# Kernel tuning notes

Hardware: AMD Instinct MI355X
Metric: run time of the kernel (lower is better)

The kernel has to match this reference:

```python
import jax, jax.numpy as jnp
import numpy as np

TOPK, NUM_CLASSES, ALPHA, BETA, EPS = 13, 80, 1.0, 6.0, 1e-9
IOU_EPS = 1e-7  # eps used inside bbox_iou (ultralytics default)


def ciou(box1, box2):
    # box1, box2: broadcastable [..., 4] in xyxy format; returns CIoU [..., 1]
    b1x1, b1y1, b1x2, b1y2 = jnp.split(box1, 4, axis=-1)
    b2x1, b2y1, b2x2, b2y2 = jnp.split(box2, 4, axis=-1)
    w1, h1 = b1x2 - b1x1, b1y2 - b1y1 + IOU_EPS
    w2, h2 = b2x2 - b2x1, b2y2 - b2y1 + IOU_EPS
    inter = (jnp.clip(jnp.minimum(b1x2, b2x2) - jnp.maximum(b1x1, b2x1), 0.0) *
             jnp.clip(jnp.minimum(b1y2, b2y2) - jnp.maximum(b1y1, b2y1), 0.0))
    union = w1 * h1 + w2 * h2 - inter + IOU_EPS
    iou = inter / union
    cw = jnp.maximum(b1x2, b2x2) - jnp.minimum(b1x1, b2x1)  # enclosing box width
    ch = jnp.maximum(b1y2, b2y2) - jnp.minimum(b1y1, b2y1)
    c2 = cw ** 2 + ch ** 2 + IOU_EPS
    rho2 = ((b2x1 + b2x2 - b1x1 - b1x2) ** 2 + (b2y1 + b2y2 - b1y1 - b1y2) ** 2) / 4.0
    v = (4.0 / np.pi ** 2) * (jnp.arctan(w2 / h2) - jnp.arctan(w1 / h1)) ** 2
    alpha = jax.lax.stop_gradient(v / (v - iou + (1.0 + IOU_EPS)))  # torch: with no_grad
    return iou - (rho2 / c2 + v * alpha)


def tal_forward(pd_scores, pd_bboxes, anc_points, gt_labels, gt_bboxes, mask_gt):
    bs, na, nc = pd_scores.shape
    nb = gt_bboxes.shape[1]
    dt = pd_scores.dtype
    mgt = mask_gt[..., 0]  # (b, nb)

    # --- select_candidates_in_gts: anchor center strictly inside gt box ---
    lt, rb = gt_bboxes[..., :2], gt_bboxes[..., 2:]
    deltas = jnp.concatenate([anc_points[None, None, :, :] - lt[:, :, None, :],
                              rb[:, :, None, :] - anc_points[None, None, :, :]], axis=-1)  # (b,nb,na,4)
    mask_in_gts = (deltas.min(-1) > EPS).astype(dt)  # (b,nb,na)
    valid = (mask_in_gts * mgt[:, :, None]) > 0  # bool (b,nb,na)

    # --- get_box_metrics: class score gather + pairwise CIoU, masked ---
    lbl = gt_labels[..., 0].astype(jnp.int32)  # (b,nb)
    scores = jnp.take_along_axis(pd_scores, lbl[:, None, :], axis=2)  # (b,na,nb)
    bbox_scores = jnp.where(valid, scores.transpose(0, 2, 1), 0.0)  # (b,nb,na)
    ov = ciou(gt_bboxes[:, :, None, :], pd_bboxes[:, None, :, :])[..., 0]  # (b,nb,na)
    overlaps = jnp.where(valid, jnp.clip(ov, 0.0), 0.0)
    align_metric = bbox_scores ** ALPHA * overlaps ** BETA

    # --- select_topk_candidates ---
    _, tk_i = jax.lax.top_k(align_metric, TOPK)  # (b,nb,TOPK)
    tk_i = jnp.where(mgt[:, :, None] > 0, tk_i, 0)  # invalid gt rows -> all idx 0 (counted >1 -> zeroed)
    flat_i = tk_i.reshape(bs * nb, TOPK)
    cnt = jnp.zeros((bs * nb, na), jnp.int32).at[jnp.arange(bs * nb)[:, None], flat_i].add(1)
    cnt = cnt.reshape(bs, nb, na)
    is_in_topk = jnp.where(cnt > 1, 0, cnt).astype(dt)
    mask_pos = is_in_topk * mask_in_gts * mgt[:, :, None]

    # --- select_highest_overlaps: resolve anchors claimed by multiple gts ---
    fg = mask_pos.sum(-2)  # (b,na)
    mask_multi = fg[:, None, :] > 1
    max_idx = overlaps.argmax(1)  # (b,na)
    is_max = jax.nn.one_hot(max_idx, nb, dtype=dt).transpose(0, 2, 1)  # (b,nb,na)
    mask_pos = jnp.where(mask_multi, is_max, mask_pos)
    fg_mask = mask_pos.sum(-2)  # (b,na)
    target_gt_idx = mask_pos.argmax(-2)  # (b,na)

    # --- get_targets ---
    flat_gt_idx = target_gt_idx + jnp.arange(bs)[:, None] * nb  # (b,na)
    target_labels = jnp.clip(lbl.reshape(-1)[flat_gt_idx], 0)
    target_bboxes = gt_bboxes.reshape(-1, 4)[flat_gt_idx]  # (b,na,4)
    target_scores = jax.nn.one_hot(target_labels, nc, dtype=dt)
    target_scores = jnp.where(fg_mask[..., None] > 0, target_scores, 0.0)

    # --- normalization of align metric ---
    align_metric = align_metric * mask_pos
    pos_align = align_metric.max(-1, keepdims=True)  # (b,nb,1)
    pos_over = (overlaps * mask_pos).max(-1, keepdims=True)
    norm = (align_metric * pos_over / (pos_align + EPS)).max(-2)[..., None]  # (b,na,1)
    target_scores = target_scores * norm
    return target_labels, target_bboxes, target_scores, fg_mask > 0, target_gt_idx


def _make_boxes(key, shape):
    kc, kw = jax.random.split(key)
    c = jax.random.uniform(kc, shape[:-1] + (2,), jnp.float32, 60.0, 580.0)
    wh = jax.random.uniform(kw, shape[:-1] + (2,), jnp.float32, 20.0, 120.0)
    return jnp.concatenate([c - wh / 2, c + wh / 2], axis=-1)


def setup_inputs() -> dict:
    key = jax.random.key(0)
    ks = jax.random.split(key, 6)
    bs, na, nc, nb = 32, 8400, 80, 64
    pd_scores = jax.random.uniform(ks[0], (bs, na, nc), jnp.float32)
    pd_bboxes = _make_boxes(ks[1], (bs, na, 4))
    anc_points = jax.random.uniform(ks[2], (na, 2), jnp.float32, 0.0, 640.0)
    gt_labels = jax.random.randint(ks[3], (bs, nb, 1), 0, nc, dtype=jnp.int32)
    gt_bboxes = _make_boxes(ks[4], (bs, nb, 4))
    mask_gt = (jax.random.uniform(ks[5], (bs, nb, 1)) < 0.8).astype(jnp.float32)
    return {"pd_scores": pd_scores, "pd_bboxes": pd_bboxes, "anc_points": anc_points,
            "gt_labels": gt_labels, "gt_bboxes": gt_bboxes, "mask_gt": mask_gt}


def reference(pd_scores, pd_bboxes, anc_points, gt_labels, gt_bboxes, mask_gt):
    return tal_forward(pd_scores, pd_bboxes, anc_points, gt_labels, gt_bboxes, mask_gt)
```

## Files before the change

### kernel.cpp

```cpp
#include <hip/hip_runtime.h>
#include <stdint.h>

#pragma clang fp contract(off)

#define BS 32
#define NB 64
#define NA 8400
#define NC 80
#define TK 13
#define QCAP 640
#define CMAX (QCAP + 32)
#define FORCED 32

typedef float floatx4 __attribute__((ext_vector_type(4)));

__device__ __forceinline__ float ciou_f(float g0, float g1, float g2, float g3,
                                        float p0, float p1, float p2, float p3) {
    const float E = 1e-7f;
    float w1 = g2 - g0, h1 = (g3 - g1) + E;
    float w2 = p2 - p0, h2 = (p3 - p1) + E;
    float iw = fminf(g2, p2) - fmaxf(g0, p0); iw = fmaxf(iw, 0.f);
    float ih = fminf(g3, p3) - fmaxf(g1, p1); ih = fmaxf(ih, 0.f);
    float inter = iw * ih;
    float uni = w1 * h1 + w2 * h2 - inter + E;
    float iou = inter / uni;
    float cw = fmaxf(g2, p2) - fminf(g0, p0);
    float ch = fmaxf(g3, p3) - fminf(g1, p1);
    float c2 = cw * cw + ch * ch + E;
    float dx = p0 + p2 - g0 - g2;
    float dy = p1 + p3 - g1 - g3;
    float rho2 = (dx * dx + dy * dy) / 4.0f;
    float da = atanf(w2 / h2) - atanf(w1 / h1);
    float v = 0.4052847345693511f * (da * da);
    float alpha = v / ((v - iou) + 1.0000001f);
    return iou - (rho2 / c2 + v * alpha);
}

__global__ __launch_bounds__(256) void k1a_scan(
    const float* __restrict__ anc,
    const float* __restrict__ gt_bboxes,
    const float* __restrict__ mask_gt,
    int* __restrict__ qcnt, int* __restrict__ qlist)
{
    int b = blockIdx.y;
    int a = blockIdx.x * 256 + threadIdx.x;
    int lane = threadIdx.x & 63;
    bool inrange = a < NA;
    float2 ap = inrange ? *(const float2*)&anc[2 * a] : make_float2(-1.f, -1.f);
    for (int j = 0; j < NB; j++) {
        int r = b * NB + j;
        float mg = mask_gt[r];
        float4 g = *(const float4*)&gt_bboxes[r * 4];
        float d0 = ap.x - g.x, d1 = ap.y - g.y, d2 = g.z - ap.x, d3 = g.w - ap.y;
        float dmin = fminf(fminf(d0, d1), fminf(d2, d3));
        bool hit = inrange && (mg > 0.f) && (dmin > 1e-9f);
        unsigned long long m = __ballot(hit);
        if (m) {
            int rank = __popcll(m & ((1ull << lane) - 1ull));
            int ldr = __ffsll((long long)m) - 1;
            int base = 0;
            if (lane == ldr) base = atomicAdd(&qcnt[r], __popcll(m));
            base = __shfl(base, ldr);
            int p = base + rank;
            if (hit && p < QCAP) qlist[r * QCAP + p] = a;
        }
    }
}

__global__ __launch_bounds__(64) void k1b_topk(
    const float* __restrict__ pd_scores,
    const float* __restrict__ pd_bboxes,
    const float* __restrict__ anc,
    const int* __restrict__ gt_labels,
    const float* __restrict__ gt_bboxes,
    const float* __restrict__ mask_gt,
    const int* __restrict__ qcnt, const int* __restrict__ qlist,
    int* __restrict__ tk_a, float* __restrict__ tk_v,
    float* __restrict__ tk_o, int* __restrict__ tk_f,
    int* __restrict__ cnt)
{
    int r = blockIdx.x;
    int b = r >> 6;
    int lane = threadIdx.x;

    if (mask_gt[r] <= 0.f) {
        if (lane < TK) {
            tk_a[r * TK + lane] = 0; tk_v[r * TK + lane] = 0.f;
            tk_o[r * TK + lane] = 0.f; tk_f[r * TK + lane] = 0;
        }
        return;
    }

    __shared__ int   ca[CMAX];
    __shared__ float cv[CMAX];
    __shared__ float co[CMAX];

    float4 g = *(const float4*)&gt_bboxes[r * 4];
    int lbl = gt_labels[r];
    int n0 = min(qcnt[r], QCAP);

    bool add = false;
    if (lane < FORCED) {
        float2 ap = *(const float2*)&anc[2 * lane];
        float d0 = ap.x - g.x, d1 = ap.y - g.y, d2 = g.z - ap.x, d3 = g.w - ap.y;
        float dmin = fminf(fminf(d0, d1), fminf(d2, d3));
        add = !(dmin > 1e-9f);
    }
    unsigned long long mb = __ballot(add);
    int pos = __popcll(mb & ((1ull << lane) - 1ull));
    if (add) { ca[n0 + pos] = lane; cv[n0 + pos] = 0.f; co[n0 + pos] = 0.f; }
    int n = n0 + __popcll(mb);

    for (int c = lane; c < n0; c += 64) {
        int a = qlist[r * QCAP + c];
        float4 p = *(const float4*)&pd_bboxes[(b * NA + a) * 4];
        float ov = fmaxf(ciou_f(g.x, g.y, g.z, g.w, p.x, p.y, p.z, p.w), 0.f);
        float sc = pd_scores[(b * NA + a) * NC + lbl];
        float o2 = ov * ov;
        ca[c] = a | (1 << 30); cv[c] = sc * (o2 * o2 * o2); co[c] = ov;
    }
    __syncthreads();

    unsigned consumed = 0;
    int wslot = 0; float wval = 0.f;
    for (int round = 0; round < TK; round++) {
        float bv = -2.f; int bgi = 0x7fffffff; int bsl = 0;
        int li = 0;
        for (int c = lane; c < n; c += 64, li++) {
            if (consumed & (1u << li)) continue;
            float v = cv[c]; int gi = ca[c] & 0x3fffffff;
            if (v > bv || (v == bv && gi < bgi)) { bv = v; bgi = gi; bsl = c; }
        }
        for (int off = 32; off; off >>= 1) {
            float v2 = __shfl_down(bv, off);
            int  gi2 = __shfl_down(bgi, off);
            int  sl2 = __shfl_down(bsl, off);
            if (v2 > bv || (v2 == bv && gi2 < bgi)) { bv = v2; bgi = gi2; bsl = sl2; }
        }
        int wsl = __shfl(bsl, 0);
        float wv = __shfl(bv, 0);
        if ((wsl & 63) == lane) consumed |= 1u << (wsl >> 6);
        if (lane == round) { wslot = wsl; wval = wv; }
    }
    if (lane < TK) {
        int packed = ca[wslot]; int a = packed & 0x3fffffff; int in = (packed >> 30) & 1;
        tk_a[r * TK + lane] = a;
        tk_v[r * TK + lane] = wval;
        tk_o[r * TK + lane] = co[wslot];
        tk_f[r * TK + lane] = in;
        if (in) atomicAdd(&cnt[b * NA + a], 1);
    }
}

__global__ void k2c_single(const int* __restrict__ tk_a, const float* __restrict__ tk_v,
                           const float* __restrict__ tk_o, const int* __restrict__ tk_f,
                           const int* __restrict__ cnt, int* __restrict__ jA,
                           float* __restrict__ av,
                           unsigned* __restrict__ posA, unsigned* __restrict__ posO,
                           int* __restrict__ mlist, int* __restrict__ mcount) {
    int c = blockIdx.x * 256 + threadIdx.x;
    if (c >= BS * NB * TK) return;
    if (!tk_f[c]) return;
    int r = c / TK; int b = r >> 6; int j = r & 63;
    int a = tk_a[c];
    int i = b * NA + a;
    if (cnt[i] == 1) {
        jA[i] = j + 1; av[i] = tk_v[c];
        atomicMax(&posA[b * NB + j], __float_as_uint(tk_v[c]));
        atomicMax(&posO[b * NB + j], __float_as_uint(tk_o[c]));
    } else {
        int old = atomicCAS(&jA[i], 0, -1);
        if (old == 0) { int p = atomicAdd(mcount, 1); mlist[p] = i; }
    }
}

__global__ __launch_bounds__(256) void k2d_multi(
    const float* __restrict__ pd_scores,
    const float* __restrict__ pd_bboxes,
    const float* __restrict__ anc,
    const int* __restrict__ gt_labels,
    const float* __restrict__ gt_bboxes,
    const float* __restrict__ mask_gt,
    const int* __restrict__ mlist, const int* __restrict__ mcount,
    int* __restrict__ jA, float* __restrict__ av,
    unsigned* __restrict__ posA, unsigned* __restrict__ posO)
{
    int wid = (blockIdx.x * 256 + threadIdx.x) >> 6;
    int lane = threadIdx.x & 63;
    int nwaves = (gridDim.x * 256) >> 6;
    int nm = *mcount;
    for (int e = wid; e < nm; e += nwaves) {
        int i = mlist[e];
        int b = i / NA, a = i - b * NA;
        float2 ap = *(const float2*)&anc[2 * a];
        int row = b * NB + lane;
        float o = 0.f;
        if (mask_gt[row] > 0.f) {
            float4 g = *(const float4*)&gt_bboxes[row * 4];
            float d0 = ap.x - g.x, d1 = ap.y - g.y, d2 = g.z - ap.x, d3 = g.w - ap.y;
            float dmin = fminf(fminf(d0, d1), fminf(d2, d3));
            if (dmin > 1e-9f) {
                float4 p = *(const float4*)&pd_bboxes[(b * NA + a) * 4];
                o = fmaxf(ciou_f(g.x, g.y, g.z, g.w, p.x, p.y, p.z, p.w), 0.f);
            }
        }
        float bv = o; int bj = lane;
        for (int off = 32; off; off >>= 1) {
            float v2 = __shfl_down(bv, off);
            int  j2 = __shfl_down(bj, off);
            if (v2 > bv || (v2 == bv && j2 < bj)) { bv = v2; bj = j2; }
        }
        if (lane == 0) {
            int lbl = gt_labels[b * NB + bj];
            float sc = pd_scores[(b * NA + a) * NC + lbl];
            float o2 = bv * bv;
            float alg = sc * (o2 * o2 * o2);
            jA[i] = bj + 1; av[i] = alg;
            atomicMax(&posA[b * NB + bj], __float_as_uint(alg));
            atomicMax(&posO[b * NB + bj], __float_as_uint(bv));
        }
    }
}

__global__ __launch_bounds__(256) void k3_final(
    const int* __restrict__ gt_labels,
    const float* __restrict__ gt_bboxes,
    const int* __restrict__ jA, const float* __restrict__ av,
    const unsigned* __restrict__ posA, const unsigned* __restrict__ posO,
    float* __restrict__ out)
{
    int t = blockIdx.x * 256 + threadIdx.x;
    int row = t / 20;
    int q = t - row * 20;
    int b = row / NA;
    int jj1 = jA[row];
    int tg = jj1 > 0 ? jj1 - 1 : 0;
    int lab = gt_labels[b * NB + tg]; lab = lab < 0 ? 0 : lab;

    float nrm = 0.f;
    if (jj1 > 0) {
        float pa = __uint_as_float(posA[b * NB + tg]);
        float po = __uint_as_float(posO[b * NB + tg]);
        nrm = (av[row] * po) / (pa + 1e-9f);
    }

    int c4 = q * 4;
    int cls = (jj1 > 0) ? lab : -1;
    floatx4 v;
    v.x = (c4 + 0 == cls) ? nrm : 0.f;
    v.y = (c4 + 1 == cls) ? nrm : 0.f;
    v.z = (c4 + 2 == cls) ? nrm : 0.f;
    v.w = (c4 + 3 == cls) ? nrm : 0.f;
    float* o_sc = out + BS * NA * 5;
    __builtin_nontemporal_store(v, (floatx4*)&o_sc[row * NC + c4]);

    if (q == 0) {
        float* o_lab  = out;
        float* o_bbox = out + BS * NA;
        float* o_fg   = out + BS * NA * (5 + NC);
        float* o_idx  = o_fg + BS * NA;
        o_lab[row] = (float)lab;
        float4 bb = *(const float4*)&gt_bboxes[(b * NB + tg) * 4];
        *(float4*)&o_bbox[row * 4] = bb;
        o_fg[row] = (jj1 > 0) ? 1.f : 0.f;
        o_idx[row] = (float)tg;
    }
}

extern "C" void kernel_launch(void* const* d_in, const int* in_sizes, int n_in,
                              void* d_out, int out_size, void* d_ws, size_t ws_size,
                              hipStream_t stream) {
    const float* pd_scores = (const float*)d_in[0];
    const float* pd_bboxes = (const float*)d_in[1];
    const float* anc       = (const float*)d_in[2];
    const int*   gt_labels = (const int*)d_in[3];
    const float* gt_bboxes = (const float*)d_in[4];
    const float* mask_gt   = (const float*)d_in[5];
    float* out = (float*)d_out;

    char* w = (char*)d_ws;
    const int NCAND = BS * NB * TK;
    char* zbase = w;
    int*      cnt  = (int*)w;      w += BS * NA * 4;
    int*      jA   = (int*)w;      w += BS * NA * 4;
    int*      qcnt = (int*)w;      w += BS * NB * 4;
    unsigned* posA = (unsigned*)w; w += BS * NB * 4;
    unsigned* posO = (unsigned*)w; w += BS * NB * 4;
    int*      mcount = (int*)w;    w += 64;
    size_t zbytes = (size_t)(w - zbase);
    float*    av   = (float*)w;    w += BS * NA * 4;
    int*      tk_a = (int*)w;      w += NCAND * 4;
    int*      tk_f = (int*)w;      w += NCAND * 4;
    float*    tk_v = (float*)w;    w += NCAND * 4;
    float*    tk_o = (float*)w;    w += NCAND * 4;
    int*      mlist = (int*)w;     w += NCAND * 4;
    int*      qlist = (int*)w;     w += BS * NB * QCAP * 4;

    hipMemsetAsync(zbase, 0, zbytes, stream);
    {
        dim3 g((NA + 255) / 256, BS);
        k1a_scan<<<g, 256, 0, stream>>>(anc, gt_bboxes, mask_gt, qcnt, qlist);
    }
    k1b_topk<<<BS * NB, 64, 0, stream>>>(pd_scores, pd_bboxes, anc, gt_labels,
                                         gt_bboxes, mask_gt, qcnt, qlist,
                                         tk_a, tk_v, tk_o, tk_f, cnt);
    k2c_single<<<(NCAND + 255) / 256, 256, 0, stream>>>(tk_a, tk_v, tk_o, tk_f,
                                                        cnt, jA, av, posA, posO,
                                                        mlist, mcount);
    k2d_multi<<<52, 256, 0, stream>>>(pd_scores, pd_bboxes, anc, gt_labels,
                                      gt_bboxes, mask_gt, mlist, mcount,
                                      jA, av, posA, posO);
    k3_final<<<BS * NA * 20 / 256, 256, 0, stream>>>(gt_labels, gt_bboxes, jA, av,
                                                     posA, posO, out);
}
```

Baseline: 263.1 us.

## Fuse all stages into one cooperative persistent kernel with grid syncs

Replaces the memset and five separate kernel launches with a single cooperative kernel of 512 blocks that zeroes the workspace itself and separates the phases with grid-wide syncs. Each block now handles four gt rows in the top-k phase, one per wave, using per-wave shared buffers. The aim is to remove launch gaps and the memset overhead. In exchange, grid.sync has its own cost, occupancy is limited by the cooperative grid size, and the output stores are no longer nontemporal.

After: 544.1 us. 107% more time.

```diff
diff --git a/kernel.cpp b/kernel.cpp
--- a/kernel.cpp
+++ b/kernel.cpp
@@ -1,16 +1,25 @@
 #include <hip/hip_runtime.h>
+#include <hip/hip_cooperative_groups.h>
 #include <stdint.h>
 
 #pragma clang fp contract(off)
+
+namespace cg = cooperative_groups;
 
 #define BS 32
 #define NB 64
 #define NA 8400
+#define NAP 8448
 #define NC 80
 #define TK 13
 #define QCAP 640
 #define CMAX (QCAP + 32)
 #define FORCED 32
+#define NBLK 512
+#define NTHR 256
+#define TTOT (NBLK * NTHR)
+#define NCAND (BS * NB * TK)
+#define ZWORDS (2 * BS * NA + 3 * BS * NB + 16)
 
 typedef float floatx4 __attribute__((ext_vector_type(4)));
 
@@ -36,229 +45,210 @@
     return iou - (rho2 / c2 + v * alpha);
 }
 
-__global__ __launch_bounds__(256) void k1a_scan(
-    const float* __restrict__ anc,
-    const float* __restrict__ gt_bboxes,
-    const float* __restrict__ mask_gt,
-    int* __restrict__ qcnt, int* __restrict__ qlist)
-{
-    int b = blockIdx.y;
-    int a = blockIdx.x * 256 + threadIdx.x;
-    int lane = threadIdx.x & 63;
-    bool inrange = a < NA;
-    float2 ap = inrange ? *(const float2*)&anc[2 * a] : make_float2(-1.f, -1.f);
-    for (int j = 0; j < NB; j++) {
-        int r = b * NB + j;
-        float mg = mask_gt[r];
-        float4 g = *(const float4*)&gt_bboxes[r * 4];
-        float d0 = ap.x - g.x, d1 = ap.y - g.y, d2 = g.z - ap.x, d3 = g.w - ap.y;
-        float dmin = fminf(fminf(d0, d1), fminf(d2, d3));
-        bool hit = inrange && (mg > 0.f) && (dmin > 1e-9f);
-        unsigned long long m = __ballot(hit);
-        if (m) {
-            int rank = __popcll(m & ((1ull << lane) - 1ull));
-            int ldr = __ffsll((long long)m) - 1;
-            int base = 0;
-            if (lane == ldr) base = atomicAdd(&qcnt[r], __popcll(m));
-            base = __shfl(base, ldr);
-            int p = base + rank;
-            if (hit && p < QCAP) qlist[r * QCAP + p] = a;
-        }
-    }
-}
-
-__global__ __launch_bounds__(64) void k1b_topk(
+__global__ __launch_bounds__(256, 2) void tal_fused(
     const float* __restrict__ pd_scores,
     const float* __restrict__ pd_bboxes,
     const float* __restrict__ anc,
     const int* __restrict__ gt_labels,
     const float* __restrict__ gt_bboxes,
     const float* __restrict__ mask_gt,
-    const int* __restrict__ qcnt, const int* __restrict__ qlist,
-    int* __restrict__ tk_a, float* __restrict__ tk_v,
-    float* __restrict__ tk_o, int* __restrict__ tk_f,
-    int* __restrict__ cnt)
+    float* __restrict__ out,
+    int* zero_base,
+    int* cnt, int* jA, int* qcnt, unsigned* posA, unsigned* posO, int* mcount,
+    float* av, int* tk_a, int* tk_f, float* tk_v, float* tk_o,
+    int* mlist, int* qlist)
 {
-    int r = blockIdx.x;
-    int b = r >> 6;
-    int lane = threadIdx.x;
-
-    if (mask_gt[r] <= 0.f) {
-        if (lane < TK) {
-            tk_a[r * TK + lane] = 0; tk_v[r * TK + lane] = 0.f;
-            tk_o[r * TK + lane] = 0.f; tk_f[r * TK + lane] = 0;
-        }
-        return;
-    }
-
-    __shared__ int   ca[CMAX];
-    __shared__ float cv[CMAX];
-    __shared__ float co[CMAX];
-
-    float4 g = *(const float4*)&gt_bboxes[r * 4];
-    int lbl = gt_labels[r];
-    int n0 = min(qcnt[r], QCAP);
-
-    bool add = false;
-    if (lane < FORCED) {
-        float2 ap = *(const float2*)&anc[2 * lane];
-        float d0 = ap.x - g.x, d1 = ap.y - g.y, d2 = g.z - ap.x, d3 = g.w - ap.y;
-        float dmin = fminf(fminf(d0, d1), fminf(d2, d3));
-        add = !(dmin > 1e-9f);
-    }
-    unsigned long long mb = __ballot(add);
-    int pos = __popcll(mb & ((1ull << lane) - 1ull));
-    if (add) { ca[n0 + pos] = lane; cv[n0 + pos] = 0.f; co[n0 + pos] = 0.f; }
-    int n = n0 + __popcll(mb);
-
-    for (int c = lane; c < n0; c += 64) {
-        int a = qlist[r * QCAP + c];
-        float4 p = *(const float4*)&pd_bboxes[(b * NA + a) * 4];
-        float ov = fmaxf(ciou_f(g.x, g.y, g.z, g.w, p.x, p.y, p.z, p.w), 0.f);
-        float sc = pd_scores[(b * NA + a) * NC + lbl];
-        float o2 = ov * ov;
-        ca[c] = a | (1 << 30); cv[c] = sc * (o2 * o2 * o2); co[c] = ov;
-    }
-    __syncthreads();
-
-    unsigned consumed = 0;
-    int wslot = 0; float wval = 0.f;
-    for (int round = 0; round < TK; round++) {
-        float bv = -2.f; int bgi = 0x7fffffff; int bsl = 0;
-        int li = 0;
-        for (int c = lane; c < n; c += 64, li++) {
-            if (consumed & (1u << li)) continue;
-            float v = cv[c]; int gi = ca[c] & 0x3fffffff;
-            if (v > bv || (v == bv && gi < bgi)) { bv = v; bgi = gi; bsl = c; }
-        }
-        for (int off = 32; off; off >>= 1) {
-            float v2 = __shfl_down(bv, off);
-            int  gi2 = __shfl_down(bgi, off);
-            int  sl2 = __shfl_down(bsl, off);
-            if (v2 > bv || (v2 == bv && gi2 < bgi)) { bv = v2; bgi = gi2; bsl = sl2; }
-        }
-        int wsl = __shfl(bsl, 0);
-        float wv = __shfl(bv, 0);
-        if ((wsl & 63) == lane) consumed |= 1u << (wsl >> 6);
-        if (lane == round) { wslot = wsl; wval = wv; }
-    }
-    if (lane < TK) {
-        int packed = ca[wslot]; int a = packed & 0x3fffffff; int in = (packed >> 30) & 1;
-        tk_a[r * TK + lane] = a;
-        tk_v[r * TK + lane] = wval;
-        tk_o[r * TK + lane] = co[wslot];
-        tk_f[r * TK + lane] = in;
-        if (in) atomicAdd(&cnt[b * NA + a], 1);
-    }
-}
-
-__global__ void k2c_single(const int* __restrict__ tk_a, const float* __restrict__ tk_v,
-                           const float* __restrict__ tk_o, const int* __restrict__ tk_f,
-                           const int* __restrict__ cnt, int* __restrict__ jA,
-                           float* __restrict__ av,
-                           unsigned* __restrict__ posA, unsigned* __restrict__ posO,
-                           int* __restrict__ mlist, int* __restrict__ mcount) {
-    int c = blockIdx.x * 256 + threadIdx.x;
-    if (c >= BS * NB * TK) return;
-    if (!tk_f[c]) return;
-    int r = c / TK; int b = r >> 6; int j = r & 63;
-    int a = tk_a[c];
-    int i = b * NA + a;
-    if (cnt[i] == 1) {
-        jA[i] = j + 1; av[i] = tk_v[c];
-        atomicMax(&posA[b * NB + j], __float_as_uint(tk_v[c]));
-        atomicMax(&posO[b * NB + j], __float_as_uint(tk_o[c]));
-    } else {
-        int old = atomicCAS(&jA[i], 0, -1);
-        if (old == 0) { int p = atomicAdd(mcount, 1); mlist[p] = i; }
-    }
-}
-
-__global__ __launch_bounds__(256) void k2d_multi(
-    const float* __restrict__ pd_scores,
-    const float* __restrict__ pd_bboxes,
-    const float* __restrict__ anc,
-    const int* __restrict__ gt_labels,
-    const float* __restrict__ gt_bboxes,
-    const float* __restrict__ mask_gt,
-    const int* __restrict__ mlist, const int* __restrict__ mcount,
-    int* __restrict__ jA, float* __restrict__ av,
-    unsigned* __restrict__ posA, unsigned* __restrict__ posO)
-{
-    int wid = (blockIdx.x * 256 + threadIdx.x) >> 6;
-    int lane = threadIdx.x & 63;
-    int nwaves = (gridDim.x * 256) >> 6;
-    int nm = *mcount;
-    for (int e = wid; e < nm; e += nwaves) {
-        int i = mlist[e];
-        int b = i / NA, a = i - b * NA;
-        float2 ap = *(const float2*)&anc[2 * a];
-        int row = b * NB + lane;
-        float o = 0.f;
-        if (mask_gt[row] > 0.f) {
-            float4 g = *(const float4*)&gt_bboxes[row * 4];
+    cg::grid_group gg = cg::this_grid();
+    const int tid = blockIdx.x * NTHR + threadIdx.x;
+    const int lane = threadIdx.x & 63;
+
+    __shared__ int   s_ca[4][CMAX];
+    __shared__ float s_cv[4][CMAX];
+    __shared__ float s_co[4][CMAX];
+
+    for (int i = tid; i < ZWORDS; i += TTOT) zero_base[i] = 0;
+    gg.sync();
+
+    for (int idx = tid; idx < BS * NAP; idx += TTOT) {
+        int b = idx / NAP; int a = idx - b * NAP;
+        bool inr = a < NA;
+        float2 ap = inr ? *(const float2*)&anc[2 * a] : make_float2(-1e9f, -1e9f);
+        for (int j = 0; j < NB; j++) {
+            int r = b * NB + j;
+            float mg = mask_gt[r];
+            float4 g = *(const float4*)&gt_bboxes[r * 4];
             float d0 = ap.x - g.x, d1 = ap.y - g.y, d2 = g.z - ap.x, d3 = g.w - ap.y;
             float dmin = fminf(fminf(d0, d1), fminf(d2, d3));
-            if (dmin > 1e-9f) {
+            bool hit = inr && (mg > 0.f) && (dmin > 1e-9f);
+            unsigned long long m = __ballot(hit);
+            if (m) {
+                int rank = __popcll(m & ((1ull << lane) - 1ull));
+                int ldr = __ffsll((long long)m) - 1;
+                int base = 0;
+                if (lane == ldr) base = atomicAdd(&qcnt[r], __popcll(m));
+                base = __shfl(base, ldr);
+                int p = base + rank;
+                if (hit && p < QCAP) qlist[r * QCAP + p] = a;
+            }
+        }
+    }
+    gg.sync();
+
+    {
+        int wv = threadIdx.x >> 6;
+        int r = blockIdx.x * 4 + wv;
+        int b = r >> 6;
+        int* ca = s_ca[wv]; float* cv = s_cv[wv]; float* co = s_co[wv];
+
+        if (mask_gt[r] <= 0.f) {
+            if (lane < TK) {
+                tk_a[r * TK + lane] = 0; tk_v[r * TK + lane] = 0.f;
+                tk_o[r * TK + lane] = 0.f; tk_f[r * TK + lane] = 0;
+            }
+        } else {
+            float4 g = *(const float4*)&gt_bboxes[r * 4];
+            int lbl = gt_labels[r];
+            int n0 = min(qcnt[r], QCAP);
+
+            bool add = false;
+            if (lane < FORCED) {
+                float2 ap = *(const float2*)&anc[2 * lane];
+                float d0 = ap.x - g.x, d1 = ap.y - g.y, d2 = g.z - ap.x, d3 = g.w - ap.y;
+                float dmin = fminf(fminf(d0, d1), fminf(d2, d3));
+                add = !(dmin > 1e-9f);
+            }
+            unsigned long long mb = __ballot(add);
+            int pos = __popcll(mb & ((1ull << lane) - 1ull));
+            if (add) { ca[n0 + pos] = lane; cv[n0 + pos] = 0.f; co[n0 + pos] = 0.f; }
+            int n = n0 + __popcll(mb);
+
+            for (int c = lane; c < n0; c += 64) {
+                int a = qlist[r * QCAP + c];
                 float4 p = *(const float4*)&pd_bboxes[(b * NA + a) * 4];
-                o = fmaxf(ciou_f(g.x, g.y, g.z, g.w, p.x, p.y, p.z, p.w), 0.f);
-            }
-        }
-        float bv = o; int bj = lane;
-        for (int off = 32; off; off >>= 1) {
-            float v2 = __shfl_down(bv, off);
-            int  j2 = __shfl_down(bj, off);
-            if (v2 > bv || (v2 == bv && j2 < bj)) { bv = v2; bj = j2; }
-        }
-        if (lane == 0) {
-            int lbl = gt_labels[b * NB + bj];
-            float sc = pd_scores[(b * NA + a) * NC + lbl];
-            float o2 = bv * bv;
-            float alg = sc * (o2 * o2 * o2);
-            jA[i] = bj + 1; av[i] = alg;
-            atomicMax(&posA[b * NB + bj], __float_as_uint(alg));
-            atomicMax(&posO[b * NB + bj], __float_as_uint(bv));
-        }
-    }
-}
-
-__global__ __launch_bounds__(256) void k3_final(
-    const int* __restrict__ gt_labels,
-    const float* __restrict__ gt_bboxes,
-    const int* __restrict__ jA, const float* __restrict__ av,
-    const unsigned* __restrict__ posA, const unsigned* __restrict__ posO,
-    float* __restrict__ out)
-{
-    int t = blockIdx.x * 256 + threadIdx.x;
-    int row = t / 20;
-    int q = t - row * 20;
-    int b = row / NA;
-    int jj1 = jA[row];
-    int tg = jj1 > 0 ? jj1 - 1 : 0;
-    int lab = gt_labels[b * NB + tg]; lab = lab < 0 ? 0 : lab;
-
-    float nrm = 0.f;
-    if (jj1 > 0) {
-        float pa = __uint_as_float(posA[b * NB + tg]);
-        float po = __uint_as_float(posO[b * NB + tg]);
-        nrm = (av[row] * po) / (pa + 1e-9f);
-    }
-
-    int c4 = q * 4;
-    int cls = (jj1 > 0) ? lab : -1;
-    floatx4 v;
-    v.x = (c4 + 0 == cls) ? nrm : 0.f;
-    v.y = (c4 + 1 == cls) ? nrm : 0.f;
-    v.z = (c4 + 2 == cls) ? nrm : 0.f;
-    v.w = (c4 + 3 == cls) ? nrm : 0.f;
+                float ov = fmaxf(ciou_f(g.x, g.y, g.z, g.w, p.x, p.y, p.z, p.w), 0.f);
+                float sc = pd_scores[(b * NA + a) * NC + lbl];
+                float o2 = ov * ov;
+                ca[c] = a | (1 << 30); cv[c] = sc * (o2 * o2 * o2); co[c] = ov;
+            }
+
+            unsigned consumed = 0;
+            int wslot = 0; float wval = 0.f;
+            for (int round = 0; round < TK; round++) {
+                float bv = -2.f; int bgi = 0x7fffffff; int bsl = 0;
+                int li = 0;
+                for (int c = lane; c < n; c += 64, li++) {
+                    if (consumed & (1u << li)) continue;
+                    float v = cv[c]; int gi = ca[c] & 0x3fffffff;
+                    if (v > bv || (v == bv && gi < bgi)) { bv = v; bgi = gi; bsl = c; }
+                }
+                for (int off = 32; off; off >>= 1) {
+                    float v2 = __shfl_down(bv, off);
+                    int  gi2 = __shfl_down(bgi, off);
+                    int  sl2 = __shfl_down(bsl, off);
+                    if (v2 > bv || (v2 == bv && gi2 < bgi)) { bv = v2; bgi = gi2; bsl = sl2; }
+                }
+                int wsl = __shfl(bsl, 0);
+                float wvv = __shfl(bv, 0);
+                if ((wsl & 63) == lane) consumed |= 1u << (wsl >> 6);
+                if (lane == round) { wslot = wsl; wval = wvv; }
+            }
+            if (lane < TK) {
+                int packed = ca[wslot]; int a = packed & 0x3fffffff; int in = (packed >> 30) & 1;
+                tk_a[r * TK + lane] = a;
+                tk_v[r * TK + lane] = wval;
+                tk_o[r * TK + lane] = co[wslot];
+                tk_f[r * TK + lane] = in;
+                if (in) atomicAdd(&cnt[b * NA + a], 1);
+            }
+        }
+    }
+    gg.sync();
+
+    for (int c = tid; c < NCAND; c += TTOT) {
+        if (!tk_f[c]) continue;
+        int r = c / TK; int b = r >> 6; int j = r & 63;
+        int a = tk_a[c];
+        int i = b * NA + a;
+        if (cnt[i] == 1) {
+            jA[i] = j + 1; av[i] = tk_v[c];
+            atomicMax(&posA[b * NB + j], __float_as_uint(tk_v[c]));
+            atomicMax(&posO[b * NB + j], __float_as_uint(tk_o[c]));
+        } else {
+            int old = atomicCAS(&jA[i], 0, -1);
+            if (old == 0) { int p = atomicAdd(mcount, 1); mlist[p] = i; }
+        }
+    }
+    gg.sync();
+
+    {
+        int wid = tid >> 6;
+        int nm = *mcount;
+        for (int e = wid; e < nm; e += TTOT / 64) {
+            int i = mlist[e];
+            int b = i / NA, a = i - b * NA;
+            float2 ap = *(const float2*)&anc[2 * a];
+            int row = b * NB + lane;
+            float o = 0.f;
+            if (mask_gt[row] > 0.f) {
+                float4 g = *(const float4*)&gt_bboxes[row * 4];
+                float d0 = ap.x - g.x, d1 = ap.y - g.y, d2 = g.z - ap.x, d3 = g.w - ap.y;
+                float dmin = fminf(fminf(d0, d1), fminf(d2, d3));
+                if (dmin > 1e-9f) {
+                    float4 p = *(const float4*)&pd_bboxes[(b * NA + a) * 4];
+                    o = fmaxf(ciou_f(g.x, g.y, g.z, g.w, p.x, p.y, p.z, p.w), 0.f);
+                }
+            }
+            float bv = o; int bj = lane;
+            for (int off = 32; off; off >>= 1) {
+                float v2 = __shfl_down(bv, off);
+                int  j2 = __shfl_down(bj, off);
+                if (v2 > bv || (v2 == bv && j2 < bj)) { bv = v2; bj = j2; }
+            }
+            if (lane == 0) {
+                int lbl = gt_labels[b * NB + bj];
+                float sc = pd_scores[(b * NA + a) * NC + lbl];
+                float o2 = bv * bv;
+                float alg = sc * (o2 * o2 * o2);
+                jA[i] = bj + 1; av[i] = alg;
+                atomicMax(&posA[b * NB + bj], __float_as_uint(alg));
+                atomicMax(&posO[b * NB + bj], __float_as_uint(bv));
+            }
+        }
+    }
+    gg.sync();
+
     float* o_sc = out + BS * NA * 5;
-    __builtin_nontemporal_store(v, (floatx4*)&o_sc[row * NC + c4]);
-
-    if (q == 0) {
-        float* o_lab  = out;
-        float* o_bbox = out + BS * NA;
-        float* o_fg   = out + BS * NA * (5 + NC);
-        float* o_idx  = o_fg + BS * NA;
+    for (int t = tid; t < BS * NA * 20; t += TTOT) {
+        int row = t / 20;
+        int q = t - row * 20;
+        int b = row / NA;
+        int jj1 = jA[row];
+        int tg = jj1 > 0 ? jj1 - 1 : 0;
+        int lab = gt_labels[b * NB + tg]; lab = lab < 0 ? 0 : lab;
+        float nrm = 0.f;
+        if (jj1 > 0) {
+            float pa = __uint_as_float(posA[b * NB + tg]);
+            float po = __uint_as_float(posO[b * NB + tg]);
+            nrm = (av[row] * po) / (pa + 1e-9f);
+        }
+        int c4 = q * 4;
+        int cls = (jj1 > 0) ? lab : -1;
+        floatx4 v;
+        v.x = (c4 + 0 == cls) ? nrm : 0.f;
+        v.y = (c4 + 1 == cls) ? nrm : 0.f;
+        v.z = (c4 + 2 == cls) ? nrm : 0.f;
+        v.w = (c4 + 3 == cls) ? nrm : 0.f;
+        *(floatx4*)&o_sc[row * NC + c4] = v;
+    }
+    float* o_lab  = out;
+    float* o_bbox = out + BS * NA;
+    float* o_fg   = out + BS * NA * (5 + NC);
+    float* o_idx  = o_fg + BS * NA;
+    for (int row = tid; row < BS * NA; row += TTOT) {
+        int b = row / NA;
+        int jj1 = jA[row];
+        int tg = jj1 > 0 ? jj1 - 1 : 0;
+        int lab = gt_labels[b * NB + tg]; lab = lab < 0 ? 0 : lab;
         o_lab[row] = (float)lab;
         float4 bb = *(const float4*)&gt_bboxes[(b * NB + tg) * 4];
         *(float4*)&o_bbox[row * 4] = bb;
@@ -279,15 +269,13 @@
     float* out = (float*)d_out;
 
     char* w = (char*)d_ws;
-    const int NCAND = BS * NB * TK;
-    char* zbase = w;
+    int*      zero_base = (int*)w;
     int*      cnt  = (int*)w;      w += BS * NA * 4;
     int*      jA   = (int*)w;      w += BS * NA * 4;
     int*      qcnt = (int*)w;      w += BS * NB * 4;
     unsigned* posA = (unsigned*)w; w += BS * NB * 4;
     unsigned* posO = (unsigned*)w; w += BS * NB * 4;
     int*      mcount = (int*)w;    w += 64;
-    size_t zbytes = (size_t)(w - zbase);
     float*    av   = (float*)w;    w += BS * NA * 4;
     int*      tk_a = (int*)w;      w += NCAND * 4;
     int*      tk_f = (int*)w;      w += NCAND * 4;
@@ -296,20 +284,16 @@
     int*      mlist = (int*)w;     w += NCAND * 4;
     int*      qlist = (int*)w;     w += BS * NB * QCAP * 4;
 
-    hipMemsetAsync(zbase, 0, zbytes, stream);
-    {
-        dim3 g((NA + 255) / 256, BS);
-        k1a_scan<<<g, 256, 0, stream>>>(anc, gt_bboxes, mask_gt, qcnt, qlist);
-    }
-    k1b_topk<<<BS * NB, 64, 0, stream>>>(pd_scores, pd_bboxes, anc, gt_labels,
-                                         gt_bboxes, mask_gt, qcnt, qlist,
-                                         tk_a, tk_v, tk_o, tk_f, cnt);
-    k2c_single<<<(NCAND + 255) / 256, 256, 0, stream>>>(tk_a, tk_v, tk_o, tk_f,
-                                                        cnt, jA, av, posA, posO,
-                                                        mlist, mcount);
-    k2d_multi<<<52, 256, 0, stream>>>(pd_scores, pd_bboxes, anc, gt_labels,
-                                      gt_bboxes, mask_gt, mlist, mcount,
-                                      jA, av, posA, posO);
-    k3_final<<<BS * NA * 20 / 256, 256, 0, stream>>>(gt_labels, gt_bboxes, jA, av,
-                                                     posA, posO, out);
+    void* args[] = {
+        (void*)&pd_scores, (void*)&pd_bboxes, (void*)&anc,
+        (void*)&gt_labels, (void*)&gt_bboxes, (void*)&mask_gt,
+        (void*)&out,
+        (void*)&zero_base,
+        (void*)&cnt, (void*)&jA, (void*)&qcnt, (void*)&posA, (void*)&posO,
+        (void*)&mcount,
+        (void*)&av, (void*)&tk_a, (void*)&tk_f, (void*)&tk_v, (void*)&tk_o,
+        (void*)&mlist, (void*)&qlist
+    };
+    hipLaunchCooperativeKernel((const void*)tal_fused, dim3(NBLK), dim3(NTHR),
+                               args, 0, stream);
 }
```
